# Kernel tuning notes

Hardware: AMD Instinct MI355X
Metric: run time of the kernel (lower is better)

## Reference

```python
import jax, jax.numpy as jnp
import numpy as np
from jax import lax

F_CNT = 64    # factories per player
U_CNT = 2048  # units per player
GRID = 16     # spatial map side after stride-3 conv on 48x48 board


def conv2d(x, w, b, stride=1, pad=1):
    return lax.conv_general_dilated(x, w, (stride, stride), [(pad, pad), (pad, pad)],
                                    dimension_numbers=('NCHW', 'OIHW', 'NCHW')) + b[None, :, None, None]


def prelu(x, a):
    return jnp.where(x > 0, x, a * x)


def linear(x, w, b):
    return x @ w.T + b


def layernorm(x, g, b, eps=1e-5):
    mu = jnp.mean(x, -1, keepdims=True)
    var = jnp.mean((x - mu) ** 2, -1, keepdims=True)
    return (x - mu) / jnp.sqrt(var + eps) * g + b


def maxpool2(x):
    return lax.reduce_window(x, -jnp.inf, lax.max, (1, 1, 2, 2), (1, 1, 2, 2), 'VALID')


def mha4(f0, u0, f1, u1, fw, fb, uw, ub, lw, lb, num_heads=2, hidden=32):
    # FourSequenceMHAttention: per head, per player, separate Q/K/V linears for
    # factories and units; sequence order is [fac_p0, units_p0, fac_p1, units_p1].
    scale = hidden ** 0.5
    heads = []
    for h in range(num_heads):
        Q, K, V = [], [], []
        for i, (f, u) in enumerate(((f0, u0), (f1, u1))):
            b0 = h * 6 + i * 3
            Q.append(linear(f, fw[b0], fb[b0]))
            K.append(linear(f, fw[b0 + 1], fb[b0 + 1]))
            V.append(linear(f, fw[b0 + 2], fb[b0 + 2]))
            Q.append(linear(u, uw[b0], ub[b0]))
            K.append(linear(u, uw[b0 + 1], ub[b0 + 1]))
            V.append(linear(u, uw[b0 + 2], ub[b0 + 2]))
        Qc = jnp.concatenate(Q, 1)
        Kc = jnp.concatenate(K, 1)
        Vc = jnp.concatenate(V, 1)
        attn = jax.nn.softmax(jnp.einsum('bqd,bkd->bqk', Qc, Kc) / scale, axis=-1)
        heads.append(jnp.einsum('bqk,bkd->bqd', attn, Vc))
    return linear(jnp.concatenate(heads, -1), lw, lb)


def scatter_mask(feat, pos, C):
    # one-hot scatter-add of per-unit features onto the 16x16 grid (batch==1)
    gm = jnp.zeros((GRID, GRID, C), feat.dtype).at[pos[:, 0], pos[:, 1]].add(feat[0])
    return jnp.transpose(gm, (2, 0, 1))[None]  # [1,C,16,16]


def _forward(fl, p0_fac_pos, p0_unit_pos, p1_fac_pos, p1_unit_pos):
    (board, p0_fac_feat, p0_unit_feat, p1_fac_feat, p1_unit_feat,
     sp_w1, sp_b1, sp_a1, sp_w2, sp_b2, sp_a2, sp_w3, sp_b3,
     enc_fac_w, enc_fac_b, enc_unit_w, enc_unit_b, enc_lin_w, enc_lin_b,
     ext_fac_w, ext_fac_b, ext_unit_w, ext_unit_b, ext_lin_w, ext_lin_b, ext_ln_g, ext_ln_b,
     v_w1, v_b1, v_a1, v_w2, v_b2, v_a2, v_lw, v_lb,
     fo_w1, fo_b1, fo_a, fo_w2, fo_b2, ro_w1, ro_b1, ro_a, ro_w2, ro_b2) = fl

    sm = prelu(conv2d(board, sp_w1, sp_b1), sp_a1)
    sm = prelu(conv2d(sm, sp_w2, sp_b2), sp_a2)
    sm = conv2d(sm, sp_w3, sp_b3, stride=3, pad=0)  # [1,24,16,16]

    def gather(pos):
        # per-unit gather of the 24-dim spatial feature at (pos_x, pos_y)
        return jnp.transpose(sm[0][:, pos[:, 0], pos[:, 1]], (1, 0))[None]  # [1,N,24]

    f0 = jnp.concatenate([p0_fac_feat, gather(p0_fac_pos)], -1)    # [1,F,31]
    u0 = jnp.concatenate([p0_unit_feat, gather(p0_unit_pos)], -1)  # [1,U,38]
    f1 = jnp.concatenate([p1_fac_feat, gather(p1_fac_pos)], -1)
    u1 = jnp.concatenate([p1_unit_feat, gather(p1_unit_pos)], -1)

    gmu0 = scatter_mask(p0_unit_feat, p0_unit_pos, 14)
    gmf0 = scatter_mask(p0_fac_feat, p0_fac_pos, 7)
    gmu1 = scatter_mask(p1_unit_feat, p1_unit_pos, 14)
    gmf1 = scatter_mask(p1_fac_feat, p1_fac_pos, 7)
    # loop prepends each team's masks: after p1 order is [u1, f1, u0, f0, spatial]
    v_map = jnp.concatenate([gmu1, gmf1, gmu0, gmf0, sm], 1)  # [1,66,16,16]

    seq = mha4(f0, u0, f1, u1, enc_fac_w, enc_fac_b, enc_unit_w, enc_unit_b, enc_lin_w, enc_lin_b)
    S0, S1, S2 = F_CNT, F_CNT + U_CNT, 2 * F_CNT + U_CNT
    for l in range(2):
        new = mha4(seq[:, :S0], seq[:, S0:S1], seq[:, S1:S2], seq[:, S2:],
                   ext_fac_w[l], ext_fac_b[l], ext_unit_w[l], ext_unit_b[l],
                   ext_lin_w[l], ext_lin_b[l])
        seq = layernorm(seq + new, ext_ln_g[l], ext_ln_b[l])

    def head2(x, w1, b1, a, w2, b2):
        return linear(prelu(linear(x, w1, b1), a), w2, b2)

    f0o = head2(seq[:, :S0], fo_w1, fo_b1, fo_a, fo_w2, fo_b2)      # [1,F,4]
    u0o = head2(seq[:, S0:S1], ro_w1, ro_b1, ro_a, ro_w2, ro_b2)    # [1,U,17]
    f1o = head2(seq[:, S1:S2], fo_w1, fo_b1, fo_a, fo_w2, fo_b2)
    u1o = head2(seq[:, S2:], ro_w1, ro_b1, ro_a, ro_w2, ro_b2)

    vm = maxpool2(prelu(conv2d(v_map, v_w1, v_b1), v_a1))  # [1,96,8,8]
    vm = maxpool2(prelu(conv2d(vm, v_w2, v_b2), v_a2))     # [1,128,4,4]
    v = jnp.tanh(vm.reshape(vm.shape[0], -1) @ v_lw.T + v_lb)  # [1,1]
    return (f0o, u0o, f1o, u1o, v)


def setup_inputs() -> dict:
    key = jax.random.key(0)
    ks = iter(jax.random.split(key, 64))

    def rn(shape, s=1.0):
        return s * jax.random.normal(next(ks), shape, dtype=jnp.float32)

    def ri(shape):
        return jax.random.randint(next(ks), shape, 0, GRID)

    a25 = lambda: jnp.full((1,), 0.25, jnp.float32)  # torch PReLU default
    inp = {
        'board': rn((1, 14, 48, 48)),
        'p0_fac_feat': rn((1, F_CNT, 7)), 'p0_unit_feat': rn((1, U_CNT, 14)),
        'p1_fac_feat': rn((1, F_CNT, 7)), 'p1_unit_feat': rn((1, U_CNT, 14)),
        'sp_w1': rn((48, 14, 3, 3), 0.05), 'sp_b1': rn((48,), 0.05), 'sp_a1': a25(),
        'sp_w2': rn((96, 48, 3, 3), 0.05), 'sp_b2': rn((96,), 0.05), 'sp_a2': a25(),
        'sp_w3': rn((24, 96, 3, 3), 0.05), 'sp_b3': rn((24,), 0.05),
        'enc_fac_w': rn((12, 32, 31), 0.05), 'enc_fac_b': rn((12, 32), 0.05),
        'enc_unit_w': rn((12, 32, 38), 0.05), 'enc_unit_b': rn((12, 32), 0.05),
        'enc_lin_w': rn((32, 64), 0.05), 'enc_lin_b': rn((32,), 0.05),
        'ext_fac_w': rn((2, 12, 32, 32), 0.05), 'ext_fac_b': rn((2, 12, 32), 0.05),
        'ext_unit_w': rn((2, 12, 32, 32), 0.05), 'ext_unit_b': rn((2, 12, 32), 0.05),
        'ext_lin_w': rn((2, 32, 64), 0.05), 'ext_lin_b': rn((2, 32), 0.05),
        'ext_ln_g': jnp.ones((2, 32), jnp.float32), 'ext_ln_b': jnp.zeros((2, 32), jnp.float32),
        'v_w1': rn((96, 66, 3, 3), 0.05), 'v_b1': rn((96,), 0.05), 'v_a1': a25(),
        'v_w2': rn((128, 96, 3, 3), 0.05), 'v_b2': rn((128,), 0.05), 'v_a2': a25(),
        'v_lw': rn((1, 128 * 16), 0.05), 'v_lb': rn((1,), 0.05),
        'fo_w1': rn((32, 32), 0.05), 'fo_b1': rn((32,), 0.05), 'fo_a': a25(),
        'fo_w2': rn((4, 32), 0.05), 'fo_b2': rn((4,), 0.05),
        'ro_w1': rn((32, 32), 0.05), 'ro_b1': rn((32,), 0.05), 'ro_a': a25(),
        'ro_w2': rn((17, 32), 0.05), 'ro_b2': rn((17,), 0.05),
        'p0_fac_pos': ri((F_CNT, 2)), 'p0_unit_pos': ri((U_CNT, 2)),
        'p1_fac_pos': ri((F_CNT, 2)), 'p1_unit_pos': ri((U_CNT, 2)),
    }
    return inp


def reference(board, p0_fac_feat, p0_unit_feat, p1_fac_feat, p1_unit_feat,
              sp_w1, sp_b1, sp_a1, sp_w2, sp_b2, sp_a2, sp_w3, sp_b3,
              enc_fac_w, enc_fac_b, enc_unit_w, enc_unit_b, enc_lin_w, enc_lin_b,
              ext_fac_w, ext_fac_b, ext_unit_w, ext_unit_b, ext_lin_w, ext_lin_b, ext_ln_g, ext_ln_b,
              v_w1, v_b1, v_a1, v_w2, v_b2, v_a2, v_lw, v_lb,
              fo_w1, fo_b1, fo_a, fo_w2, fo_b2, ro_w1, ro_b1, ro_a, ro_w2, ro_b2,
              p0_fac_pos, p0_unit_pos, p1_fac_pos, p1_unit_pos):
    fl = (board, p0_fac_feat, p0_unit_feat, p1_fac_feat, p1_unit_feat,
          sp_w1, sp_b1, sp_a1, sp_w2, sp_b2, sp_a2, sp_w3, sp_b3,
          enc_fac_w, enc_fac_b, enc_unit_w, enc_unit_b, enc_lin_w, enc_lin_b,
          ext_fac_w, ext_fac_b, ext_unit_w, ext_unit_b, ext_lin_w, ext_lin_b, ext_ln_g, ext_ln_b,
          v_w1, v_b1, v_a1, v_w2, v_b2, v_a2, v_lw, v_lb,
          fo_w1, fo_b1, fo_a, fo_w2, fo_b2, ro_w1, ro_b1, ro_a, ro_w2, ro_b2)
    return _forward(fl, p0_fac_pos, p0_unit_pos, p1_fac_pos, p1_unit_pos)
```

## Files before the change

kernel.cpp:

```cpp
#include <hip/hip_runtime.h>
#include <hip/hip_bf16.h>

#define SEQ 4224
#define KSPLIT 11
#define KITERS 6
typedef unsigned int uint;
typedef unsigned short ushort;
typedef __attribute__((ext_vector_type(8))) short bf16x8;
typedef __attribute__((ext_vector_type(4))) float f32x4;

__device__ __forceinline__ float prelu_f(float x, float a){ return x > 0.f ? x : a*x; }

__device__ __forceinline__ ushort bfr(float x){
  uint u = __float_as_uint(x);
  u = (u + 0x7fffu + ((u>>16)&1u)) >> 16;
  return (ushort)u;
}
__device__ __forceinline__ uint pkbf(float a, float b){
  __hip_bfloat162 h2 = __float22bfloat162_rn(make_float2(a,b));
  union { __hip_bfloat162 h; uint u; } cv; cv.h = h2; return cv.u;
}

#define QSCALE 0.25505607190037247f

struct MegaParams {
  const float *board,*p0f,*p0u,*p1f,*p1u;
  const float *sp_w1,*sp_b1,*sp_a1,*sp_w2,*sp_b2,*sp_a2,*sp_w3,*sp_b3;
  const float *enc_fac_w,*enc_fac_b,*enc_unit_w,*enc_unit_b,*enc_lin_w,*enc_lin_b;
  const float *ext_fac_w,*ext_fac_b,*ext_unit_w,*ext_unit_b,*ext_lin_w,*ext_lin_b,*ext_ln_g,*ext_ln_b;
  const float *v_w1,*v_b1,*v_a1,*v_w2,*v_b2,*v_a2,*v_lw,*v_lb;
  const float *fo_w1,*fo_b1,*fo_a,*fo_w2,*fo_b2,*ro_w1,*ro_b1,*ro_a,*ro_w2,*ro_b2;
  const int *p0fp,*p0up,*p1fp,*p1up;
  float* out;
  float *sm1,*sm2,*sm,*F0,*U0,*F1,*U1;
  ushort *q16,*k16,*vt16;
  float *Hp,*aux,*seqA,*seqB,*vmap,*vp1,*vp2;
};

template<int CIN, int HW>
__device__ __forceinline__ void conv_item(int cg_, int pxb, int tid,
    const float* __restrict__ in, const float* __restrict__ w,
    const float* __restrict__ bias, const float* __restrict__ alpha,
    float* __restrict__ out, float* SF){
  float* Ws = SF;
  float* Bs = SF + 4*CIN*9;
  for (int idx=tid; idx<4*CIN*9; idx+=256) Ws[idx] = w[cg_*4*CIN*9 + idx];
  if (tid<4) Bs[tid] = bias[cg_*4+tid];
  __syncthreads();
  int p = pxb*256 + tid;
  int x = p % HW, y = p / HW;
  float a = alpha[0];
  float acc[4];
  #pragma unroll
  for (int c=0;c<4;++c) acc[c]=Bs[c];
  #pragma unroll 2
  for (int i=0;i<CIN;++i){
    const float* ip = in + i*HW*HW;
    float win[9];
    #pragma unroll
    for (int ky=0;ky<3;++ky){
      int yy = y+ky-1;
      #pragma unroll
      for (int kx=0;kx<3;++kx){
        int xx = x+kx-1;
        bool ok = ((unsigned)yy < (unsigned)HW) && ((unsigned)xx < (unsigned)HW);
        win[ky*3+kx] = ok ? ip[yy*HW+xx] : 0.f;
      }
    }
    #pragma unroll
    for (int c=0;c<4;++c){
      const float* wp = &Ws[(c*CIN+i)*9];
      #pragma unroll
      for (int k=0;k<9;++k) acc[c] += win[k]*wp[k];
    }
  }
  #pragma unroll
  for (int c=0;c<4;++c)
    out[(cg_*4+c)*HW*HW + p] = prelu_f(acc[c], a);
}

__device__ __forceinline__ void convs3_item(int cg_, int tid,
    const float* __restrict__ in, const float* __restrict__ w,
    const float* __restrict__ bias, float* __restrict__ out, float* SF){
  float* Ws = SF;
  for (int idx=tid; idx<1728; idx+=256) Ws[idx] = w[cg_*1728 + idx];
  __syncthreads();
  int x = tid&15, y = tid>>4;
  float a0 = bias[2*cg_], a1 = bias[2*cg_+1];
  const float* ip0 = in + y*144 + x*3;
  #pragma unroll 4
  for (int i=0;i<96;++i){
    const float* ip = ip0 + i*2304;
    float win[9];
    #pragma unroll
    for (int ky=0;ky<3;++ky)
      #pragma unroll
      for (int kx=0;kx<3;++kx) win[ky*3+kx] = ip[ky*48+kx];
    const float* w0 = &Ws[i*9];
    const float* w1 = &Ws[864 + i*9];
    #pragma unroll
    for (int k=0;k<9;++k){ a0 += win[k]*w0[k]; a1 += win[k]*w1[k]; }
  }
  out[(2*cg_)*256 + y*16 + x] = a0;
  out[(2*cg_+1)*256 + y*16 + x] = a1;
}

__device__ __forceinline__ void gather_item(int e, const MegaParams& P){
  if (e>=SEQ) return;
  const float* feat; const int* pos; float* dst; int nf, n;
  if (e<64){ n=e; feat=P.p0f+n*7; pos=P.p0fp; dst=P.F0+n*31; nf=7; }
  else if (e<2112){ n=e-64; feat=P.p0u+n*14; pos=P.p0up; dst=P.U0+(size_t)n*38; nf=14; }
  else if (e<2176){ n=e-2112; feat=P.p1f+n*7; pos=P.p1fp; dst=P.F1+n*31; nf=7; }
  else { n=e-2176; feat=P.p1u+n*14; pos=P.p1up; dst=P.U1+(size_t)n*38; nf=14; }
  for (int c=0;c<nf;++c) dst[c]=feat[c];
  int px = pos[2*n], py = pos[2*n+1];
  const float* s = P.sm + px*16 + py;
  #pragma unroll
  for (int c=0;c<24;++c) dst[nf+c] = s[c*256];
}

__device__ __forceinline__ void scatter_item(int e, const MegaParams& P){
  if (e>=SEQ) return;
  const float* feat; const int* pos; int n, ch0, C;
  if (e<2048){ n=e; feat=P.p1u+n*14; pos=P.p1up; ch0=0; C=14; }
  else if (e<2112){ n=e-2048; feat=P.p1f+n*7; pos=P.p1fp; ch0=14; C=7; }
  else if (e<4160){ n=e-2112; feat=P.p0u+n*14; pos=P.p0up; ch0=21; C=14; }
  else { n=e-4160; feat=P.p0f+n*7; pos=P.p0fp; ch0=35; C=7; }
  int off = pos[2*n]*16 + pos[2*n+1];
  for (int c=0;c<C;++c) atomicAdd(&P.vmap[(ch0+c)*256 + off], feat[c]);
}

__device__ __forceinline__ void qkv_item(int blk, int tid,
    const float* x0, const float* x1, const float* x2, const float* x3,
    int ind_f, int ind_u,
    const float* fw, const float* fb, const float* uw, const float* ub,
    ushort* Q16, ushort* K16, ushort* VT16, float* SF){
  float* Xs = SF;
  float* Ws = SF + 2560;
  float* Bs = SF + 3840;
  int chunk = blk % 66;
  int hm = blk / 66;
  int m = hm >> 1, h = hm & 1;
  const float* xb; int ind, isfac, pl;
  if (chunk==0){ xb=x0; ind=ind_f; isfac=1; pl=0; }
  else if (chunk<=32){ xb=x1 + (size_t)(chunk-1)*64*ind_u; ind=ind_u; isfac=0; pl=0; }
  else if (chunk==33){ xb=x2; ind=ind_f; isfac=1; pl=1; }
  else { xb=x3 + (size_t)(chunk-34)*64*ind_u; ind=ind_u; isfac=0; pl=1; }
  int b0 = h*6 + pl*3 + m;
  const float* w = (isfac? fw:uw) + (size_t)b0*32*ind;
  const float* bias = (isfac? fb:ub) + b0*32;
  {
    int r = tid>>2, seg = tid&3;
    const float* xr = xb + (size_t)r*ind;
    #pragma unroll
    for (int j=0;j<10;++j){ int c = seg*10+j; Xs[r*40+c] = (c<ind) ? xr[c] : 0.f; }
    int o = tid>>3, sg = tid&7;
    const float* wr = w + (size_t)o*ind;
    #pragma unroll
    for (int j=0;j<5;++j){ int c = sg*5+j; Ws[o*40+c] = (c<ind) ? wr[c] : 0.f; }
    if (tid<32) Bs[tid]=bias[tid];
  }
  __syncthreads();
  int og = tid&7, rg = tid>>3;
  const float4* Xs4 = (const float4*)Xs;
  const float4* Ws4 = (const float4*)Ws;
  float acc[2][4];
  #pragma unroll
  for (int k=0;k<4;++k){ float b = Bs[og+8*k]; acc[0][k]=b; acc[1][k]=b; }
  #pragma unroll
  for (int d4=0; d4<10; ++d4){
    float4 xa = Xs4[rg*10+d4];
    float4 xb2 = Xs4[(rg+32)*10+d4];
    #pragma unroll
    for (int k=0;k<4;++k){
      float4 wv = Ws4[(og+8*k)*10+d4];
      acc[0][k] += xa.x*wv.x + xa.y*wv.y + xa.z*wv.z + xa.w*wv.w;
      acc[1][k] += xb2.x*wv.x + xb2.y*wv.y + xb2.z*wv.z + xb2.w*wv.w;
    }
  }
  if (m==0){
    #pragma unroll
    for (int j=0;j<2;++j){
      int r = rg + 32*j;
      ushort* base = Q16 + ((size_t)h*SEQ + chunk*64 + r)*32;
      #pragma unroll
      for (int k=0;k<4;++k) base[og+8*k] = bfr(acc[j][k]*QSCALE);
    }
  } else if (m==1){
    #pragma unroll
    for (int j=0;j<2;++j){
      int r = rg + 32*j;
      ushort* base = K16 + ((size_t)h*SEQ + chunk*64 + r)*32;
      #pragma unroll
      for (int k=0;k<4;++k) base[og+8*k] = bfr(acc[j][k]);
    }
  } else {
    #pragma unroll
    for (int k=0;k<4;++k){
      ushort* base = VT16 + ((size_t)h*32 + og+8*k)*SEQ + chunk*64;
      #pragma unroll
      for (int j=0;j<2;++j) base[rg+32*j] = bfr(acc[j][k]);
    }
  }
}

__device__ __forceinline__ void flash_item(int item, int tid,
    const ushort* Q16, const ushort* K16, const ushort* VT16,
    float* Hpart, float* aux, ushort* SU){
  ushort* KsB = SU;
  ushort* VTB = SU + 5120;
  ushort* PlB = SU + 10240;
  int qb = item % 66, h = (item/66)&1, ks = item/132;
  int wv = tid>>6, l = tid&63, lq = l&15, g = l>>4;
  const ushort* Qh = Q16 + (size_t)h*SEQ*32;
  const ushort* Kh = K16 + (size_t)h*SEQ*32;
  const ushort* VTh = VT16 + (size_t)h*32*SEQ;

  bf16x8 qf = *(const bf16x8*)(Qh + (size_t)(qb*64 + wv*16 + lq)*32 + g*8);

  int krow = tid>>2, kc8 = (tid&3)*8;
  int vd = tid>>3, vk8 = (tid&7)*8;

  f32x4 o0 = {0.f,0.f,0.f,0.f}, o1 = {0.f,0.f,0.f,0.f};
  float mr = -1e30f, lrow = 0.f;

  int kt0 = ks*KITERS;
  bf16x8 kpre = *(const bf16x8*)(Kh + (size_t)(kt0*64 + krow)*32 + kc8);
  bf16x8 vpre = *(const bf16x8*)(VTh + (size_t)vd*SEQ + kt0*64 + vk8);
  *(bf16x8*)&KsB[0*2560 + krow*40 + kc8] = kpre;
  *(bf16x8*)&VTB[0*2560 + vd*80 + vk8] = vpre;

  for (int it=0; it<KITERS; ++it){
    int pb = it&1;
    if (it+1 < KITERS){
      kpre = *(const bf16x8*)(Kh + (size_t)((kt0+it+1)*64 + krow)*32 + kc8);
      vpre = *(const bf16x8*)(VTh + (size_t)vd*SEQ + (kt0+it+1)*64 + vk8);
    }
    __syncthreads();
    f32x4 z = {0.f,0.f,0.f,0.f};
    f32x4 sT[4];
    #pragma unroll
    for (int m=0;m<4;++m){
      bf16x8 kf = *(const bf16x8*)&KsB[pb*2560 + (16*m+lq)*40 + g*8];
      sT[m] = __builtin_amdgcn_mfma_f32_16x16x32_bf16(kf, qf, z, 0, 0, 0);
    }
    float tm = -1e30f;
    #pragma unroll
    for (int m=0;m<4;++m)
      tm = fmaxf(tm, fmaxf(fmaxf(sT[m][0],sT[m][1]), fmaxf(sT[m][2],sT[m][3])));
    tm = fmaxf(tm, __shfl_xor(tm,16));
    tm = fmaxf(tm, __shfl_xor(tm,32));
    float mnew = fmaxf(mr, tm);
    float rsc = exp2f(mr - mnew);
    float ts = 0.f;
    #pragma unroll
    for (int m=0;m<4;++m){
      #pragma unroll
      for (int r=0;r<4;++r){ float p = exp2f(sT[m][r]-mnew); sT[m][r]=p; ts+=p; }
    }
    ts += __shfl_xor(ts,16); ts += __shfl_xor(ts,32);
    lrow = lrow*rsc + ts; mr = mnew;
    #pragma unroll
    for (int m=0;m<4;++m){
      uint2 pw; pw.x = pkbf(sT[m][0],sT[m][1]); pw.y = pkbf(sT[m][2],sT[m][3]);
      *(uint2*)&PlB[wv*1152 + lq*72 + 16*m + g*4] = pw;
    }
    float rr0 = __shfl(rsc, (g<<2)+0);
    float rr1 = __shfl(rsc, (g<<2)+1);
    float rr2 = __shfl(rsc, (g<<2)+2);
    float rr3 = __shfl(rsc, (g<<2)+3);
    o0[0]*=rr0; o0[1]*=rr1; o0[2]*=rr2; o0[3]*=rr3;
    o1[0]*=rr0; o1[1]*=rr1; o1[2]*=rr2; o1[3]*=rr3;
    #pragma unroll
    for (int s=0;s<2;++s){
      bf16x8 pf = *(const bf16x8*)&PlB[wv*1152 + lq*72 + s*32 + g*8];
      bf16x8 vf0 = *(const bf16x8*)&VTB[pb*2560 + lq*80 + s*32 + g*8];
      bf16x8 vf1 = *(const bf16x8*)&VTB[pb*2560 + (lq+16)*80 + s*32 + g*8];
      o0 = __builtin_amdgcn_mfma_f32_16x16x32_bf16(pf, vf0, o0, 0, 0, 0);
      o1 = __builtin_amdgcn_mfma_f32_16x16x32_bf16(pf, vf1, o1, 0, 0, 0);
    }
    if (it+1 < KITERS){
      *(bf16x8*)&KsB[(pb^1)*2560 + krow*40 + kc8] = kpre;
      *(bf16x8*)&VTB[(pb^1)*2560 + vd*80 + vk8] = vpre;
    }
  }
  int qg0 = qb*64 + wv*16;
  #pragma unroll
  for (int r=0;r<4;++r){
    size_t row = (size_t)ks*SEQ + qg0 + g*4 + r;
    Hpart[row*64 + h*32 + lq]      = o0[r];
    Hpart[row*64 + h*32 + lq + 16] = o1[r];
  }
  if (g==0){
    float* ap = aux + ((size_t)(ks*2+h)*SEQ + qg0 + lq)*2;
    ap[0]=mr; ap[1]=lrow;
  }
}

__device__ __forceinline__ float combine_row(const float* Hp, const float* aux, int s, int d){
  int hh = d>>5;
  float m[KSPLIT], li[KSPLIT];
  #pragma unroll
  for (int p=0;p<KSPLIT;++p){
    const float* ap = aux + ((size_t)(p*2+hh)*SEQ + s)*2;
    m[p]=ap[0]; li[p]=ap[1];
  }
  float ms = m[0];
  #pragma unroll
  for (int p=1;p<KSPLIT;++p) ms = fmaxf(ms, m[p]);
  float den = 0.f, hv = 0.f;
  #pragma unroll
  for (int p=0;p<KSPLIT;++p){
    float w = exp2f(m[p]-ms);
    den += li[p]*w;
    hv  += Hp[(size_t)p*SEQ*64 + (size_t)s*64 + d]*w;
  }
  return hv/den;
}

__device__ __forceinline__ void outlin_item(int blk, int tid,
    const float* Hp, const float* aux, const float* lw, const float* lb,
    const float* seqin, const float* g, const float* b, float* seqout,
    bool LN, float* SF){
  float* Ls = SF;
  float* Hc = SF + 2176;
  int s0 = blk*8;
  for (int idx=tid; idx<2048; idx+=256){ int o=idx>>6, d=idx&63; Ls[o*68+d]=lw[idx]; }
  for (int idx=tid; idx<512; idx+=256){
    int sl = idx>>6, d = idx&63;
    Hc[sl*68+d] = combine_row(Hp, aux, s0+sl, d);
  }
  __syncthreads();
  int o = tid&31, sl = tid>>5;
  const float4* H4 = (const float4*)&Hc[sl*68];
  const float4* L4 = (const float4*)&Ls[o*68];
  float acc = lb[o] + (LN ? seqin[(s0+sl)*32+o] : 0.f);
  #pragma unroll
  for (int d4=0; d4<16; ++d4){
    float4 hv = H4[d4], lv = L4[d4];
    acc += hv.x*lv.x + hv.y*lv.y + hv.z*lv.z + hv.w*lv.w;
  }
  if (LN){
    float sum=acc;
    #pragma unroll
    for (int off=1; off<32; off<<=1) sum += __shfl_xor(sum,off);
    float mu = sum*0.03125f;
    float dv = acc-mu;
    float vs = dv*dv;
    #pragma unroll
    for (int off=1; off<32; off<<=1) vs += __shfl_xor(vs,off);
    float rstd = rsqrtf(vs*0.03125f + 1e-5f);
    seqout[(s0+sl)*32+o] = dv*rstd*g[o] + b[o];
  } else {
    seqout[(s0+sl)*32+o] = acc;
  }
}

__device__ __forceinline__ void qkv_layer(const MegaParams& P, int layer, int blk, int tid, float* SF){
  if (layer==0)
    qkv_item(blk, tid, P.F0,P.U0,P.F1,P.U1, 31,38,
        P.enc_fac_w,P.enc_fac_b,P.enc_unit_w,P.enc_unit_b, P.q16,P.k16,P.vt16, SF);
  else if (layer==1)
    qkv_item(blk, tid, P.seqA, P.seqA+64*32, P.seqA+2112*32, P.seqA+2176*32, 32,32,
        P.ext_fac_w,P.ext_fac_b,P.ext_unit_w,P.ext_unit_b, P.q16,P.k16,P.vt16, SF);
  else
    qkv_item(blk, tid, P.seqB, P.seqB+64*32, P.seqB+2112*32, P.seqB+2176*32, 32,32,
        P.ext_fac_w+12288,P.ext_fac_b+384,P.ext_unit_w+12288,P.ext_unit_b+384, P.q16,P.k16,P.vt16, SF);
}
__device__ __forceinline__ void outlin_layer(const MegaParams& P, int layer, int blk, int tid, float* SF){
  if (layer==0)
    outlin_item(blk,tid,P.Hp,P.aux,P.enc_lin_w,P.enc_lin_b,nullptr,nullptr,nullptr,P.seqA,false,SF);
  else if (layer==1)
    outlin_item(blk,tid,P.Hp,P.aux,P.ext_lin_w,P.ext_lin_b,P.seqA,P.ext_ln_g,P.ext_ln_b,P.seqB,true,SF);
  else
    outlin_item(blk,tid,P.Hp,P.aux,P.ext_lin_w+2048,P.ext_lin_b+32,P.seqB,P.ext_ln_g+32,P.ext_ln_b+32,P.seqA,true,SF);
}

__device__ __forceinline__ void vconv1_item(int item2, int tid, const MegaParams& P, float* SF){
  float* In = SF;
  float* Wc = SF + 6336;
  int c = item2>>2, q = item2&3;
  int y0 = q*4;
  const float4* in4 = (const float4*)P.vmap;
  float4* In4 = (float4*)In;
  for (int idx4=tid; idx4<1584; idx4+=256){
    int i = idx4/24, rem = idx4 - i*24;
    int r = rem>>2, x4 = rem&3;
    int y = y0 - 1 + r;
    float4 v;
    if ((unsigned)y < 16u) v = in4[i*64 + y*4 + x4];
    else { v.x=v.y=v.z=v.w=0.f; }
    In4[idx4] = v;
  }
  for (int idx=tid; idx<594; idx+=256) Wc[idx] = P.v_w1[c*594 + idx];
  __syncthreads();
  if (tid<64){
    int x = tid & 15, ry = tid >> 4;
    float a = P.v_a1[0];
    float acc = P.v_b1[c];
    for (int i=0;i<66;++i){
      const float* base = &In[i*96 + ry*16];
      const float* wp = &Wc[i*9];
      #pragma unroll
      for (int ky=0;ky<3;++ky){
        const float* row = base + ky*16;
        #pragma unroll
        for (int kx=0;kx<3;++kx){
          int xx = x+kx-1;
          float v = ((unsigned)xx<16u) ? row[xx] : 0.f;
          acc += v*wp[ky*3+kx];
        }
      }
    }
    acc = prelu_f(acc, a);
    float mx = fmaxf(acc, __shfl_xor(acc,1));
    mx = fmaxf(mx, __shfl_xor(mx,16));
    if (((x&1)==0) && ((ry&1)==0))
      P.vp1[c*64 + (q*2 + (ry>>1))*8 + (x>>1)] = mx;
  }
}

__device__ __forceinline__ void vconv2_item(int c, int tid, const MegaParams& P, float* SF){
  float* In = SF;
  float* Ws = SF + 6144;
  const float4* in4 = (const float4*)P.vp1;
  float4* In4 = (float4*)In;
  for (int idx4=tid; idx4<1536; idx4+=256) In4[idx4] = in4[idx4];
  for (int idx=tid; idx<864; idx+=256) Ws[idx] = P.v_w2[c*864 + idx];
  __syncthreads();
  if (tid<64){
    int x = tid&7, y = tid>>3;
    float acc = P.v_b2[c];
    for (int i=0;i<96;++i){
      const float* base = &In[i*64];
      const float* wp = &Ws[i*9];
      #pragma unroll
      for (int ky=0;ky<3;++ky){
        int yy = y+ky-1;
        #pragma unroll
        for (int kx=0;kx<3;++kx){
          int xx = x+kx-1;
          bool ok = ((unsigned)yy<8u) && ((unsigned)xx<8u);
          float v = ok ? base[yy*8+xx] : 0.f;
          acc += v*wp[ky*3+kx];
        }
      }
    }
    acc = prelu_f(acc, P.v_a2[0]);
    float mx = fmaxf(acc, __shfl_xor(acc,1));
    mx = fmaxf(mx, __shfl_xor(mx,8));
    if (((x&1)==0) && ((y&1)==0))
      P.vp2[c*16 + (y>>1)*4 + (x>>1)] = mx;
  }
}

__device__ __forceinline__ void vfinal_item(int tid, const MegaParams& P, float* SF){
  float* red = SF;
  float s=0.f;
  for (int i=tid;i<2048;i+=256) s += P.vp2[i]*P.v_lw[i];
  red[tid]=s; __syncthreads();
  for (int k=128;k>0;k>>=1){ if (tid<k) red[tid]+=red[tid+k]; __syncthreads(); }
  if (tid==0) P.out[70144] = tanhf(red[0]+P.v_lb[0]);
}

__device__ __forceinline__ void head_item(int e, const MegaParams& P){
  if (e>=SEQ) return;
  const float *w1,*b1,*w2,*b2; float a; int od; float* dst;
  float* out = P.out;
  if (e<64){ w1=P.fo_w1;b1=P.fo_b1;a=P.fo_a[0];w2=P.fo_w2;b2=P.fo_b2;od=4; dst=out + e*4; }
  else if (e<2112){ w1=P.ro_w1;b1=P.ro_b1;a=P.ro_a[0];w2=P.ro_w2;b2=P.ro_b2;od=17; dst=out + 256 + (size_t)(e-64)*17; }
  else if (e<2176){ w1=P.fo_w1;b1=P.fo_b1;a=P.fo_a[0];w2=P.fo_w2;b2=P.fo_b2;od=4; dst=out + 35072 + (e-2112)*4; }
  else { w1=P.ro_w1;b1=P.ro_b1;a=P.ro_a[0];w2=P.ro_w2;b2=P.ro_b2;od=17; dst=out + 35328 + (size_t)(e-2176)*17; }
  float x[32];
  #pragma unroll
  for (int i=0;i<32;++i) x[i]=P.seqA[(size_t)e*32+i];
  float hbuf[32];
  #pragma unroll
  for (int j=0;j<32;++j){
    float acc=b1[j];
    #pragma unroll
    for (int i=0;i<32;++i) acc+=w1[j*32+i]*x[i];
    hbuf[j]=prelu_f(acc,a);
  }
  for (int k=0;k<od;++k){
    float acc=b2[k];
    #pragma unroll
    for (int j=0;j<32;++j) acc+=w2[k*32+j]*hbuf[j];
    dst[k]=acc;
  }
}

__global__ __launch_bounds__(256) void k_conv1z(MegaParams P){
  __shared__ __align__(16) float SF[512];
  if (blockIdx.x < 108)
    conv_item<14,48>(blockIdx.x/9, blockIdx.x%9, threadIdx.x, P.board,P.sp_w1,P.sp_b1,P.sp_a1,P.sm1,SF);
  else
    P.vmap[(blockIdx.x-108)*256+threadIdx.x] = 0.f;
}
__global__ __launch_bounds__(256) void k_conv2(MegaParams P){
  __shared__ __align__(16) float SF[1736];
  conv_item<48,48>(blockIdx.x/9, blockIdx.x%9, threadIdx.x, P.sm1,P.sp_w2,P.sp_b2,P.sp_a2,P.sm2,SF);
}
__global__ __launch_bounds__(256) void k_convs3(MegaParams P){
  __shared__ __align__(16) float SF[1728];
  convs3_item(blockIdx.x, threadIdx.x, P.sm2,P.sp_w3,P.sp_b3,P.sm,SF);
}
__global__ __launch_bounds__(256) void k_gsc(MegaParams P){
  int b = blockIdx.x;
  if (b<17) gather_item(b*256+threadIdx.x, P);
  else if (b<41){ int idx=(b-17)*256+threadIdx.x; P.vmap[42*256+idx] = P.sm[idx]; }
  else scatter_item((b-41)*256+threadIdx.x, P);
}
__global__ __launch_bounds__(256) void k_qkv0_vc1(MegaParams P){
  __shared__ __align__(16) float SF[6930];
  if (blockIdx.x < 396) qkv_layer(P, 0, blockIdx.x, threadIdx.x, SF);
  else vconv1_item(blockIdx.x-396, threadIdx.x, P, SF);
}
__global__ __launch_bounds__(256) void k_flash0_vc2(MegaParams P){
  __shared__ __align__(16) char SM[29696];
  if (blockIdx.x < 1452) flash_item(blockIdx.x, threadIdx.x, P.q16,P.k16,P.vt16,P.Hp,P.aux,(ushort*)SM);
  else vconv2_item(blockIdx.x-1452, threadIdx.x, P, (float*)SM);
}
__global__ __launch_bounds__(256) void k_outlin0_vf(MegaParams P){
  __shared__ __align__(16) float SF[2720];
  if (blockIdx.x < 528) outlin_layer(P, 0, blockIdx.x, threadIdx.x, SF);
  else vfinal_item(threadIdx.x, P, SF);
}
__global__ __launch_bounds__(256) void k_qkv(MegaParams P, int layer){
  __shared__ __align__(16) float SF[3904];
  qkv_layer(P, layer, blockIdx.x, threadIdx.x, SF);
}
__global__ __launch_bounds__(256) void k_flash(MegaParams P){
  __shared__ __align__(16) char SM[29696];
  flash_item(blockIdx.x, threadIdx.x, P.q16,P.k16,P.vt16,P.Hp,P.aux,(ushort*)SM);
}
__global__ __launch_bounds__(256) void k_outlin(MegaParams P, int layer){
  __shared__ __align__(16) float SF[2720];
  outlin_layer(P, layer, blockIdx.x, threadIdx.x, SF);
}
__global__ __launch_bounds__(256) void k_head(MegaParams P){ head_item(blockIdx.x*256+threadIdx.x, P); }

extern "C" void kernel_launch(void* const* d_in, const int* in_sizes, int n_in,
                              void* d_out, int out_size, void* d_ws, size_t ws_size,
                              hipStream_t stream){
  (void)in_sizes; (void)n_in; (void)out_size; (void)ws_size;
  MegaParams P;
  P.board=(const float*)d_in[0];
  P.p0f=(const float*)d_in[1]; P.p0u=(const float*)d_in[2];
  P.p1f=(const float*)d_in[3]; P.p1u=(const float*)d_in[4];
  P.sp_w1=(const float*)d_in[5]; P.sp_b1=(const float*)d_in[6]; P.sp_a1=(const float*)d_in[7];
  P.sp_w2=(const float*)d_in[8]; P.sp_b2=(const float*)d_in[9]; P.sp_a2=(const float*)d_in[10];
  P.sp_w3=(const float*)d_in[11]; P.sp_b3=(const float*)d_in[12];
  P.enc_fac_w=(const float*)d_in[13]; P.enc_fac_b=(const float*)d_in[14];
  P.enc_unit_w=(const float*)d_in[15]; P.enc_unit_b=(const float*)d_in[16];
  P.enc_lin_w=(const float*)d_in[17]; P.enc_lin_b=(const float*)d_in[18];
  P.ext_fac_w=(const float*)d_in[19]; P.ext_fac_b=(const float*)d_in[20];
  P.ext_unit_w=(const float*)d_in[21]; P.ext_unit_b=(const float*)d_in[22];
  P.ext_lin_w=(const float*)d_in[23]; P.ext_lin_b=(const float*)d_in[24];
  P.ext_ln_g=(const float*)d_in[25]; P.ext_ln_b=(const float*)d_in[26];
  P.v_w1=(const float*)d_in[27]; P.v_b1=(const float*)d_in[28]; P.v_a1=(const float*)d_in[29];
  P.v_w2=(const float*)d_in[30]; P.v_b2=(const float*)d_in[31]; P.v_a2=(const float*)d_in[32];
  P.v_lw=(const float*)d_in[33]; P.v_lb=(const float*)d_in[34];
  P.fo_w1=(const float*)d_in[35]; P.fo_b1=(const float*)d_in[36]; P.fo_a=(const float*)d_in[37];
  P.fo_w2=(const float*)d_in[38]; P.fo_b2=(const float*)d_in[39];
  P.ro_w1=(const float*)d_in[40]; P.ro_b1=(const float*)d_in[41]; P.ro_a=(const float*)d_in[42];
  P.ro_w2=(const float*)d_in[43]; P.ro_b2=(const float*)d_in[44];
  P.p0fp=(const int*)d_in[45]; P.p0up=(const int*)d_in[46];
  P.p1fp=(const int*)d_in[47]; P.p1up=(const int*)d_in[48];
  P.out = (float*)d_out;

  float* W = (float*)d_ws;
  P.sm1 = W;
  P.sm2 = P.sm1 + 110592;
  P.sm  = P.sm2 + 221184;
  P.F0  = P.sm + 6144;
  P.U0  = P.F0 + 1984;
  P.F1  = P.U0 + 77824;
  P.U1  = P.F1 + 1984;
  P.q16 = (ushort*)(P.U1 + 77824);
  P.k16 = P.q16 + 2*SEQ*32;
  P.vt16 = P.k16 + 2*SEQ*32;
  P.Hp  = (float*)(P.vt16 + 2*SEQ*32);
  P.aux = P.Hp + KSPLIT*SEQ*64;
  P.seqA= P.aux + KSPLIT*2*SEQ*2;
  P.seqB= P.seqA + SEQ*32;
  P.vmap= P.seqB + SEQ*32;
  P.vp1 = P.vmap + 66*256;
  P.vp2 = P.vp1 + 96*64;

  k_conv1z<<<150,256,0,stream>>>(P);
  k_conv2<<<216,256,0,stream>>>(P);
  k_convs3<<<12,256,0,stream>>>(P);
  k_gsc<<<58,256,0,stream>>>(P);
  k_qkv0_vc1<<<780,256,0,stream>>>(P);
  k_flash0_vc2<<<1580,256,0,stream>>>(P);
  k_outlin0_vf<<<529,256,0,stream>>>(P);
  k_qkv<<<396,256,0,stream>>>(P,1);
  k_flash<<<1452,256,0,stream>>>(P);
  k_outlin<<<528,256,0,stream>>>(P,1);
  k_qkv<<<396,256,0,stream>>>(P,2);
  k_flash<<<1452,256,0,stream>>>(P);
  k_outlin<<<528,256,0,stream>>>(P,2);
  k_head<<<17,256,0,stream>>>(P);
}
```

Before: 364.0 us.

## Load flash K/V fragments directly from global and rebalance fused value-branch kernels

The flash attention item no longer stages K and V^T tiles through double-buffered LDS with block-wide barriers. Each wave now reads its MFMA fragments straight from global memory, and only the per-wave P tile stays in LDS. The value-branch conv2 and final stages move into the outlin0 and qkv1 launches so the flash kernel runs alone with a small LDS footprint. The spatial conv2 is also split into 2 output channels per block instead of 4, doubling the grid. This removes barriers and LDS traffic and may raise occupancy, at the cost of redundant global and L2 reads of K/V across the four waves.

```diff
diff --git a/kernel.cpp b/kernel.cpp
--- a/kernel.cpp
+++ b/kernel.cpp
@@ -37,22 +37,22 @@
   float *Hp,*aux,*seqA,*seqB,*vmap,*vp1,*vp2;
 };
 
-template<int CIN, int HW>
+template<int CIN, int HW, int CPT>
 __device__ __forceinline__ void conv_item(int cg_, int pxb, int tid,
     const float* __restrict__ in, const float* __restrict__ w,
     const float* __restrict__ bias, const float* __restrict__ alpha,
     float* __restrict__ out, float* SF){
   float* Ws = SF;
-  float* Bs = SF + 4*CIN*9;
-  for (int idx=tid; idx<4*CIN*9; idx+=256) Ws[idx] = w[cg_*4*CIN*9 + idx];
-  if (tid<4) Bs[tid] = bias[cg_*4+tid];
+  float* Bs = SF + CPT*CIN*9;
+  for (int idx=tid; idx<CPT*CIN*9; idx+=256) Ws[idx] = w[cg_*CPT*CIN*9 + idx];
+  if (tid<CPT) Bs[tid] = bias[cg_*CPT+tid];
   __syncthreads();
   int p = pxb*256 + tid;
   int x = p % HW, y = p / HW;
   float a = alpha[0];
-  float acc[4];
-  #pragma unroll
-  for (int c=0;c<4;++c) acc[c]=Bs[c];
+  float acc[CPT];
+  #pragma unroll
+  for (int c=0;c<CPT;++c) acc[c]=Bs[c];
   #pragma unroll 2
   for (int i=0;i<CIN;++i){
     const float* ip = in + i*HW*HW;
@@ -68,15 +68,15 @@
       }
     }
     #pragma unroll
-    for (int c=0;c<4;++c){
+    for (int c=0;c<CPT;++c){
       const float* wp = &Ws[(c*CIN+i)*9];
       #pragma unroll
       for (int k=0;k<9;++k) acc[c] += win[k]*wp[k];
     }
   }
   #pragma unroll
-  for (int c=0;c<4;++c)
-    out[(cg_*4+c)*HW*HW + p] = prelu_f(acc[c], a);
+  for (int c=0;c<CPT;++c)
+    out[(cg_*CPT+c)*HW*HW + p] = prelu_f(acc[c], a);
 }
 
 __device__ __forceinline__ void convs3_item(int cg_, int tid,
@@ -204,46 +204,37 @@
   }
 }
 
-__device__ __forceinline__ void flash_item(int item, int tid,
+__device__ __forceinline__ void flash_item2(int item, int tid,
     const ushort* Q16, const ushort* K16, const ushort* VT16,
-    float* Hpart, float* aux, ushort* SU){
-  ushort* KsB = SU;
-  ushort* VTB = SU + 5120;
-  ushort* PlB = SU + 10240;
+    float* Hpart, float* aux, ushort* PlAll){
   int qb = item % 66, h = (item/66)&1, ks = item/132;
   int wv = tid>>6, l = tid&63, lq = l&15, g = l>>4;
   const ushort* Qh = Q16 + (size_t)h*SEQ*32;
   const ushort* Kh = K16 + (size_t)h*SEQ*32;
   const ushort* VTh = VT16 + (size_t)h*32*SEQ;
+  ushort* Pl = PlAll + wv*1152;
 
   bf16x8 qf = *(const bf16x8*)(Qh + (size_t)(qb*64 + wv*16 + lq)*32 + g*8);
-
-  int krow = tid>>2, kc8 = (tid&3)*8;
-  int vd = tid>>3, vk8 = (tid&7)*8;
+  const ushort* vrow0 = VTh + (size_t)lq*SEQ;
+  const ushort* vrow1 = VTh + (size_t)(lq+16)*SEQ;
 
   f32x4 o0 = {0.f,0.f,0.f,0.f}, o1 = {0.f,0.f,0.f,0.f};
   float mr = -1e30f, lrow = 0.f;
-
   int kt0 = ks*KITERS;
-  bf16x8 kpre = *(const bf16x8*)(Kh + (size_t)(kt0*64 + krow)*32 + kc8);
-  bf16x8 vpre = *(const bf16x8*)(VTh + (size_t)vd*SEQ + kt0*64 + vk8);
-  *(bf16x8*)&KsB[0*2560 + krow*40 + kc8] = kpre;
-  *(bf16x8*)&VTB[0*2560 + vd*80 + vk8] = vpre;
 
   for (int it=0; it<KITERS; ++it){
-    int pb = it&1;
-    if (it+1 < KITERS){
-      kpre = *(const bf16x8*)(Kh + (size_t)((kt0+it+1)*64 + krow)*32 + kc8);
-      vpre = *(const bf16x8*)(VTh + (size_t)vd*SEQ + (kt0+it+1)*64 + vk8);
-    }
-    __syncthreads();
+    int kt = kt0 + it;
+    const ushort* Kt = Kh + (size_t)kt*64*32 + lq*32 + g*8;
+    bf16x8 kf0 = *(const bf16x8*)(Kt);
+    bf16x8 kf1 = *(const bf16x8*)(Kt + 16*32);
+    bf16x8 kf2 = *(const bf16x8*)(Kt + 32*32);
+    bf16x8 kf3 = *(const bf16x8*)(Kt + 48*32);
     f32x4 z = {0.f,0.f,0.f,0.f};
     f32x4 sT[4];
-    #pragma unroll
-    for (int m=0;m<4;++m){
-      bf16x8 kf = *(const bf16x8*)&KsB[pb*2560 + (16*m+lq)*40 + g*8];
-      sT[m] = __builtin_amdgcn_mfma_f32_16x16x32_bf16(kf, qf, z, 0, 0, 0);
-    }
+    sT[0] = __builtin_amdgcn_mfma_f32_16x16x32_bf16(kf0, qf, z, 0, 0, 0);
+    sT[1] = __builtin_amdgcn_mfma_f32_16x16x32_bf16(kf1, qf, z, 0, 0, 0);
+    sT[2] = __builtin_amdgcn_mfma_f32_16x16x32_bf16(kf2, qf, z, 0, 0, 0);
+    sT[3] = __builtin_amdgcn_mfma_f32_16x16x32_bf16(kf3, qf, z, 0, 0, 0);
     float tm = -1e30f;
     #pragma unroll
     for (int m=0;m<4;++m)
@@ -263,7 +254,7 @@
     #pragma unroll
     for (int m=0;m<4;++m){
       uint2 pw; pw.x = pkbf(sT[m][0],sT[m][1]); pw.y = pkbf(sT[m][2],sT[m][3]);
-      *(uint2*)&PlB[wv*1152 + lq*72 + 16*m + g*4] = pw;
+      *(uint2*)&Pl[lq*72 + 16*m + g*4] = pw;
     }
     float rr0 = __shfl(rsc, (g<<2)+0);
     float rr1 = __shfl(rsc, (g<<2)+1);
@@ -271,17 +262,14 @@
     float rr3 = __shfl(rsc, (g<<2)+3);
     o0[0]*=rr0; o0[1]*=rr1; o0[2]*=rr2; o0[3]*=rr3;
     o1[0]*=rr0; o1[1]*=rr1; o1[2]*=rr2; o1[3]*=rr3;
+    int c0 = kt*64;
     #pragma unroll
     for (int s=0;s<2;++s){
-      bf16x8 pf = *(const bf16x8*)&PlB[wv*1152 + lq*72 + s*32 + g*8];
-      bf16x8 vf0 = *(const bf16x8*)&VTB[pb*2560 + lq*80 + s*32 + g*8];
-      bf16x8 vf1 = *(const bf16x8*)&VTB[pb*2560 + (lq+16)*80 + s*32 + g*8];
+      bf16x8 pf  = *(const bf16x8*)&Pl[lq*72 + s*32 + g*8];
+      bf16x8 vf0 = *(const bf16x8*)(vrow0 + c0 + s*32 + g*8);
+      bf16x8 vf1 = *(const bf16x8*)(vrow1 + c0 + s*32 + g*8);
       o0 = __builtin_amdgcn_mfma_f32_16x16x32_bf16(pf, vf0, o0, 0, 0, 0);
       o1 = __builtin_amdgcn_mfma_f32_16x16x32_bf16(pf, vf1, o1, 0, 0, 0);
-    }
-    if (it+1 < KITERS){
-      *(bf16x8*)&KsB[(pb^1)*2560 + krow*40 + kc8] = kpre;
-      *(bf16x8*)&VTB[(pb^1)*2560 + vd*80 + vk8] = vpre;
     }
   }
   int qg0 = qb*64 + wv*16;
@@ -493,13 +481,13 @@
 __global__ __launch_bounds__(256) void k_conv1z(MegaParams P){
   __shared__ __align__(16) float SF[512];
   if (blockIdx.x < 108)
-    conv_item<14,48>(blockIdx.x/9, blockIdx.x%9, threadIdx.x, P.board,P.sp_w1,P.sp_b1,P.sp_a1,P.sm1,SF);
+    conv_item<14,48,4>(blockIdx.x/9, blockIdx.x%9, threadIdx.x, P.board,P.sp_w1,P.sp_b1,P.sp_a1,P.sm1,SF);
   else
     P.vmap[(blockIdx.x-108)*256+threadIdx.x] = 0.f;
 }
 __global__ __launch_bounds__(256) void k_conv2(MegaParams P){
-  __shared__ __align__(16) float SF[1736];
-  conv_item<48,48>(blockIdx.x/9, blockIdx.x%9, threadIdx.x, P.sm1,P.sp_w2,P.sp_b2,P.sp_a2,P.sm2,SF);
+  __shared__ __align__(16) float SF[872];
+  conv_item<48,48,2>(blockIdx.x/9, blockIdx.x%9, threadIdx.x, P.sm1,P.sp_w2,P.sp_b2,P.sp_a2,P.sm2,SF);
 }
 __global__ __launch_bounds__(256) void k_convs3(MegaParams P){
   __shared__ __align__(16) float SF[1728];
@@ -516,23 +504,23 @@
   if (blockIdx.x < 396) qkv_layer(P, 0, blockIdx.x, threadIdx.x, SF);
   else vconv1_item(blockIdx.x-396, threadIdx.x, P, SF);
 }
-__global__ __launch_bounds__(256) void k_flash0_vc2(MegaParams P){
-  __shared__ __align__(16) char SM[29696];
-  if (blockIdx.x < 1452) flash_item(blockIdx.x, threadIdx.x, P.q16,P.k16,P.vt16,P.Hp,P.aux,(ushort*)SM);
-  else vconv2_item(blockIdx.x-1452, threadIdx.x, P, (float*)SM);
-}
-__global__ __launch_bounds__(256) void k_outlin0_vf(MegaParams P){
-  __shared__ __align__(16) float SF[2720];
+__global__ __launch_bounds__(256) void k_flash(MegaParams P){
+  __shared__ __align__(16) ushort Pl[4*16*72];
+  flash_item2(blockIdx.x, threadIdx.x, P.q16,P.k16,P.vt16,P.Hp,P.aux,Pl);
+}
+__global__ __launch_bounds__(256) void k_outlin0_vc2(MegaParams P){
+  __shared__ __align__(16) float SF[7008];
   if (blockIdx.x < 528) outlin_layer(P, 0, blockIdx.x, threadIdx.x, SF);
+  else vconv2_item(blockIdx.x-528, threadIdx.x, P, SF);
+}
+__global__ __launch_bounds__(256) void k_qkv1_vf(MegaParams P){
+  __shared__ __align__(16) float SF[3904];
+  if (blockIdx.x < 396) qkv_layer(P, 1, blockIdx.x, threadIdx.x, SF);
   else vfinal_item(threadIdx.x, P, SF);
 }
 __global__ __launch_bounds__(256) void k_qkv(MegaParams P, int layer){
   __shared__ __align__(16) float SF[3904];
   qkv_layer(P, layer, blockIdx.x, threadIdx.x, SF);
-}
-__global__ __launch_bounds__(256) void k_flash(MegaParams P){
-  __shared__ __align__(16) char SM[29696];
-  flash_item(blockIdx.x, threadIdx.x, P.q16,P.k16,P.vt16,P.Hp,P.aux,(ushort*)SM);
 }
 __global__ __launch_bounds__(256) void k_outlin(MegaParams P, int layer){
   __shared__ __align__(16) float SF[2720];
@@ -589,13 +577,13 @@
   P.vp2 = P.vp1 + 96*64;
 
   k_conv1z<<<150,256,0,stream>>>(P);
-  k_conv2<<<216,256,0,stream>>>(P);
+  k_conv2<<<432,256,0,stream>>>(P);
   k_convs3<<<12,256,0,stream>>>(P);
   k_gsc<<<58,256,0,stream>>>(P);
   k_qkv0_vc1<<<780,256,0,stream>>>(P);
-  k_flash0_vc2<<<1580,256,0,stream>>>(P);
-  k_outlin0_vf<<<529,256,0,stream>>>(P);
-  k_qkv<<<396,256,0,stream>>>(P,1);
+  k_flash<<<1452,256,0,stream>>>(P);
+  k_outlin0_vc2<<<656,256,0,stream>>>(P);
+  k_qkv1_vf<<<397,256,0,stream>>>(P);
   k_flash<<<1452,256,0,stream>>>(P);
   k_outlin<<<528,256,0,stream>>>(P,1);
   k_qkv<<<396,256,0,stream>>>(P,2);
```

Result: slower. 391.5 us (+7.6%).
